# Performance work log

Hardware: AMD Instinct MI355X
Metric: run time of the kernel (lower is better)

Reference implementation:

```python
import jax, jax.numpy as jnp
import numpy as np

NEG_INF = -1e30  # safe stand-in for -inf so grads stay finite
LEAKY = 0.1      # leaky_hmm_coefficient passed to ChainFunction.apply

B, T, D = 32, 500, 2048   # batch, frames, num pdfs
S, E = 2048, 65536        # denominator graph: states, arcs


def setup_inputs() -> dict:
    key = jax.random.key(0)
    k1, k2, k3, k4, k5 = jax.random.split(key, 5)
    x = jax.random.normal(k1, (B, T, D), dtype=jnp.float32)  # nnet outputs (log-space)
    from_state = jax.random.randint(k2, (E,), 0, S)
    to_state = jax.random.randint(k3, (E,), 0, S)
    pdf_ids = jax.random.randint(k4, (E,), 0, D)
    # arc log-weights (negative, like normalized FST weights)
    log_weights = -2.0 * jax.random.uniform(k5, (E,), dtype=jnp.float32)
    log_init = jnp.full((S,), -np.log(float(S)), dtype=jnp.float32)   # uniform initial
    log_final = jnp.zeros((S,), dtype=jnp.float32)                    # all states final
    return {
        "x": x,
        "log_weights": log_weights,
        "log_init": log_init,
        "log_final": log_final,
        "from_state": from_state,
        "to_state": to_state,
        "pdf_ids": pdf_ids,
    }


def _segment_logsumexp(scores, seg_ids, num_segments):
    # scores: [E, B]; logsumexp per destination state -> [S, B]
    m = jax.ops.segment_max(scores, seg_ids, num_segments=num_segments)
    m = jnp.maximum(m, NEG_INF)  # empty segments -> finite sentinel
    sums = jax.ops.segment_sum(jnp.exp(scores - m[seg_ids]), seg_ids,
                               num_segments=num_segments)
    return m + jnp.log(jnp.maximum(sums, 1e-30))


def reference(x, log_weights, log_init, log_final, from_state, to_state, pdf_ids):
    # LF-MMI chain forward recursion (log domain) over the denominator graph,
    # with leaky-HMM transitions (prob. LEAKY of jumping to any state ~ init dist).
    Bv = x.shape[0]
    Sv = log_init.shape[0]
    log_leaky = jnp.log(jnp.float32(LEAKY))

    def step(alpha, xt):  # alpha: [S, B] log-probs, xt: [B, D]
        # leaky-HMM: alpha <- logaddexp(alpha, log_leaky + init * total_mass)
        tot = jax.scipy.special.logsumexp(alpha, axis=0)           # [B]
        alpha = jnp.logaddexp(alpha, log_leaky + log_init[:, None] + tot[None, :])
        # arc scores: alpha[src] + arc weight + frame pdf score
        scores = alpha[from_state] + log_weights[:, None] + xt[:, pdf_ids].T  # [E, B]
        new_alpha = _segment_logsumexp(scores, to_state, Sv)        # [S, B]
        return new_alpha, None

    alpha0 = jnp.broadcast_to(log_init[:, None], (Sv, Bv))
    alphaT, _ = jax.lax.scan(step, alpha0, jnp.swapaxes(x, 0, 1))  # scan over T
    objf = jax.scipy.special.logsumexp(alphaT + log_final[:, None], axis=0)  # [B]
    return -jnp.sum(objf)  # Energy returns -objf
```

## Files before the change

kernel.cpp:

```cpp
#include <hip/hip_runtime.h>
#include <cstdint>

#define NS 2048
#define NE 65536
#define ND 2048
#define NB 32
#define NT 500
#define NGROUPS 32
#define ELLCAP (2*NE)
#define LEAKYF 0.1f
#define NBG 16
#define NSP 16

#define WS_COUNTS 0
#define WS_CURSOR 8192
#define WS_WIDTHS 16384
#define WS_GBASE  16640
#define WS_ALBUF  20480
#define WS_ARC    544768

typedef float __attribute__((ext_vector_type(2))) f2v;

__device__ __forceinline__ void ld2_l3(const float2* p0, const float2* p1,
                                       float2& r0, float2& r1) {
    f2v a, b;
    asm volatile("global_load_dwordx2 %0, %2, off sc0 sc1\n\t"
                 "global_load_dwordx2 %1, %3, off sc0 sc1\n\t"
                 "s_waitcnt vmcnt(0)"
                 : "=&v"(a), "=&v"(b) : "v"(p0), "v"(p1) : "memory");
    r0 = make_float2(a.x, a.y); r1 = make_float2(b.x, b.y);
}
__device__ __forceinline__ void st2_l3(float2* p, float2 v) {
    f2v d; d.x = v.x; d.y = v.y;
    asm volatile("global_store_dwordx2 %0, %1, off sc0 sc1"
                 :: "v"(p), "v"(d) : "memory");
}

__global__ void k_init(const float* __restrict__ log_init, float* albuf, float* out,
                       uint32_t* counts, uint32_t* cursor, uint4* arcp) {
    int tid = blockIdx.x * blockDim.x + threadIdx.x;
    int n = blockDim.x * gridDim.x;
    for (int i = tid; i < NS; i += n) { counts[i] = 0u; cursor[i] = 0u; }
    for (int i = tid; i < ELLCAP; i += n) arcp[i] = make_uint4(0u, 0u, 0u, 0u);
    float2* ab = reinterpret_cast<float2*>(albuf);
    for (int i = tid; i < NBG * NS; i += n) {
        int s = i & (NS - 1);
        float a = __expf(log_init[s]);
        ab[i]            = make_float2(a, a);
        ab[NBG * NS + i] = make_float2(-1.f, -1.f);
    }
    if (tid == 0) out[0] = 0.0f;
}

__global__ void k_count(const int* __restrict__ to_state, uint32_t* counts) {
    int e = blockIdx.x * blockDim.x + threadIdx.x;
    if (e < NE) atomicAdd(&counts[to_state[e]], 1u);
}

__global__ void k_widths(const uint32_t* __restrict__ counts, uint32_t* widths, uint32_t* gbase) {
    int g = threadIdx.x;
    if (g < NGROUPS) {
        uint32_t w = 0u;
        for (int i = 0; i < 64; ++i) w = max(w, counts[g*64 + i]);
        widths[g] = w;
    }
    __syncthreads();
    if (threadIdx.x == 0) {
        uint32_t acc = 0u;
        for (int g2 = 0; g2 < NGROUPS; ++g2) { gbase[g2] = acc; acc += widths[g2] * 64u; }
        gbase[NGROUPS] = acc;
    }
}

__global__ void k_scatter(const int* __restrict__ from_state, const int* __restrict__ to_state,
                          const int* __restrict__ pdf_ids, const float* __restrict__ log_w,
                          const float* __restrict__ log_init,
                          const uint32_t* __restrict__ gbase, uint32_t* cursor, uint4* arcp) {
    int e = blockIdx.x * blockDim.x + threadIdx.x;
    if (e >= NE) return;
    int s = to_state[e];
    int g = s >> 6;
    uint32_t slot = atomicAdd(&cursor[s], 1u);
    uint32_t pos = gbase[g] + slot * 64u + (uint32_t)(s & 63);
    int fs = from_state[e];
    uint32_t meta = (uint32_t)fs | ((uint32_t)pdf_ids[e] << 16);
    float w  = __expf(log_w[e]);
    float w2 = LEAKYF * __expf(log_init[fs]) * w;
    arcp[pos] = make_uint4(meta, __float_as_uint(w), __float_as_uint(w2), 0u);
}

__global__ __launch_bounds__(1024, 1) void k_fwd(
    const float* __restrict__ x, const float* __restrict__ log_final,
    const uint4* __restrict__ arc, const uint32_t* __restrict__ widths,
    const uint32_t* __restrict__ gbase,
    float* albuf, float* out)
{
    __shared__ __align__(16) float2 e2[NS];
    __shared__ __align__(16) float2 Xs[2 * ND];
    __shared__ __align__(16) float2 pt[16 * 64];
    __shared__ __align__(16) float2 red[16];

    const int tid  = threadIdx.x;
    const int bg   = blockIdx.x & 15;
    const int sp   = blockIdx.x >> 4;
    const int lane = tid & 63;
    const int wid  = tid >> 6;
    const int gsel = wid >> 3;
    const int wsl  = wid & 7;
    const int g    = sp * 2 + gsel;

    const float* x0 = x + (size_t)(bg * 2)     * NT * ND;
    const float* x1 = x + (size_t)(bg * 2 + 1) * NT * ND;

    Xs[tid]        = make_float2(__expf(x0[tid]),        __expf(x1[tid]));
    Xs[tid + 1024] = make_float2(__expf(x0[tid + 1024]), __expf(x1[tid + 1024]));

    const int wd = (int)widths[g];
    const uint4* ap = arc + gbase[g] + lane;
    float2* albuf2 = reinterpret_cast<float2*>(albuf);

    float C0 = 0.f, C1 = 0.f;

    for (int t = 0; t < NT; ++t) {
        const int par = t & 1;
        const float2* cbuf = albuf2 + ((size_t)par * NBG + bg) * NS;
        float2*       nbuf = albuf2 + ((size_t)(par ^ 1) * NBG + bg) * NS;
        float2* Xcur = Xs + (size_t)par * ND;
        float2* Xnxt = Xs + (size_t)(par ^ 1) * ND;
        const uint32_t sexp = (uint32_t)((t >> 1) & 1);

        float2 A0, A1;
        for (;;) {
            ld2_l3(cbuf + tid, cbuf + tid + 1024, A0, A1);
            uint32_t m = ((__float_as_uint(A0.x) >> 31) ^ sexp)
                       | ((__float_as_uint(A0.y) >> 31) ^ sexp)
                       | ((__float_as_uint(A1.x) >> 31) ^ sexp)
                       | ((__float_as_uint(A1.y) >> 31) ^ sexp);
            if (m == 0u) break;
            __builtin_amdgcn_s_sleep(1);
        }
        A0.x = fabsf(A0.x); A0.y = fabsf(A0.y);
        A1.x = fabsf(A1.x); A1.y = fabsf(A1.y);

        float pa0, pa1, pb0, pb1;
        const bool pf = (t + 1 < NT);
        if (pf) {
            const size_t o = (size_t)(t + 1) * ND;
            pa0 = x0[o + tid];        pb0 = x1[o + tid];
            pa1 = x0[o + tid + 1024]; pb1 = x1[o + tid + 1024];
        }

        e2[tid]        = A0;
        e2[tid + 1024] = A1;
        float u0 = A0.x + A1.x, u1 = A0.y + A1.y;
        #pragma unroll
        for (int off = 32; off > 0; off >>= 1) {
            u0 += __shfl_down(u0, off, 64);
            u1 += __shfl_down(u1, off, 64);
        }
        if (lane == 0) red[wid] = make_float2(u0, u1);
        __syncthreads();

        float T0 = 0.f, T1 = 0.f;
        #pragma unroll
        for (int j = 0; j < 16; ++j) { float2 q = red[j]; T0 += q.x; T1 += q.y; }
        const float i0 = 1.0f / T0, i1 = 1.0f / T1;
        if (tid == 0) { C0 += __logf(T0); C1 += __logf(T1); }

        float2 acc = make_float2(0.f, 0.f);
        for (int i = wsl; i < wd; i += 8) {
            uint4 A = ap[(size_t)i * 64];
            const float w  = __uint_as_float(A.y);
            const float w2 = __uint_as_float(A.z);
            const int src = (int)(A.x & 0xFFFFu);
            const int pdf = (int)(A.x >> 16);
            float2 ev = e2[src];
            float2 xv = Xcur[pdf];
            acc.x = fmaf(xv.x, fmaf(ev.x * i0, w, w2), acc.x);
            acc.y = fmaf(xv.y, fmaf(ev.y * i1, w, w2), acc.y);
        }
        pt[wid * 64 + lane] = acc;
        if (pf) {
            Xnxt[tid]        = make_float2(__expf(pa0), __expf(pb0));
            Xnxt[tid + 1024] = make_float2(__expf(pa1), __expf(pb1));
        }
        __syncthreads();

        if (wsl == 0) {
            float2 r = pt[(gsel * 8) * 64 + lane];
            #pragma unroll
            for (int k = 1; k < 8; ++k) {
                float2 q = pt[(gsel * 8 + k) * 64 + lane];
                r.x += q.x; r.y += q.y;
            }
            const float sg = (((t + 1) >> 1) & 1) ? -1.f : 1.f;
            st2_l3(nbuf + sp * 128 + gsel * 64 + lane,
                   make_float2(r.x * sg, r.y * sg));
        }
    }

    if (sp == 0) {
        const float2* fbuf = albuf2 + (size_t)bg * NS;
        const uint32_t sexp = (uint32_t)((NT >> 1) & 1);
        float2 A0, A1;
        for (;;) {
            ld2_l3(fbuf + tid, fbuf + tid + 1024, A0, A1);
            uint32_t m = ((__float_as_uint(A0.x) >> 31) ^ sexp)
                       | ((__float_as_uint(A0.y) >> 31) ^ sexp)
                       | ((__float_as_uint(A1.x) >> 31) ^ sexp)
                       | ((__float_as_uint(A1.y) >> 31) ^ sexp);
            if (m == 0u) break;
            __builtin_amdgcn_s_sleep(1);
        }
        A0.x = fabsf(A0.x); A0.y = fabsf(A0.y);
        A1.x = fabsf(A1.x); A1.y = fabsf(A1.y);
        float f0 = __expf(log_final[tid]);
        float f1 = __expf(log_final[tid + 1024]);
        float u0 = A0.x * f0 + A1.x * f1;
        float u1 = A0.y * f0 + A1.y * f1;
        #pragma unroll
        for (int off = 32; off > 0; off >>= 1) {
            u0 += __shfl_down(u0, off, 64);
            u1 += __shfl_down(u1, off, 64);
        }
        if (lane == 0) red[wid] = make_float2(u0, u1);
        __syncthreads();
        if (tid == 0) {
            float t0 = 0.f, t1 = 0.f;
            #pragma unroll
            for (int j = 0; j < 16; ++j) { t0 += red[j].x; t1 += red[j].y; }
            atomicAdd(out, -(__logf(t0) + C0) - (__logf(t1) + C1));
        }
    }
}

extern "C" void kernel_launch(void* const* d_in, const int* in_sizes, int n_in,
                              void* d_out, int out_size, void* d_ws, size_t ws_size,
                              hipStream_t stream) {
    const float* x         = (const float*)d_in[0];
    const float* log_w     = (const float*)d_in[1];
    const float* log_init  = (const float*)d_in[2];
    const float* log_final = (const float*)d_in[3];
    const int*   from_st   = (const int*)d_in[4];
    const int*   to_st     = (const int*)d_in[5];
    const int*   pdf_ids   = (const int*)d_in[6];
    float* out = (float*)d_out;

    uint8_t* ws = (uint8_t*)d_ws;
    uint32_t* counts = (uint32_t*)(ws + WS_COUNTS);
    uint32_t* cursor = (uint32_t*)(ws + WS_CURSOR);
    uint32_t* widths = (uint32_t*)(ws + WS_WIDTHS);
    uint32_t* gbase  = (uint32_t*)(ws + WS_GBASE);
    float*    albuf  = (float*)(ws + WS_ALBUF);
    uint4*    arc    = (uint4*)(ws + WS_ARC);

    k_init   <<<512, 256, 0, stream>>>(log_init, albuf, out, counts, cursor, arc);
    k_count  <<<NE/256, 256, 0, stream>>>(to_st, counts);
    k_widths <<<1, 64, 0, stream>>>(counts, widths, gbase);
    k_scatter<<<NE/256, 256, 0, stream>>>(from_st, to_st, pdf_ids, log_w, log_init,
                                          gbase, cursor, arc);
    k_fwd    <<<NSP*NBG, 1024, 0, stream>>>(x, log_final, arc, widths, gbase,
                                            albuf, out);
}
```

Baseline: 2.010 ms.

## Interleave two independent batch chains per block to hide cross-block sync latency

Each persistent block now owns one 64-state group and handles two batch-pair chains in turn within every time step, instead of two state groups for one batch pair. While the block works on one chain, the other chain's alpha slice can be produced by the other blocks, so spin-wait time is meant to overlap with useful work. The grid stays at 256 blocks, now arranged as 32 state splits by 8 batch quads. This doubles the shared-memory X buffers and the number of block barriers per step, and each block writes 64 states per chain rather than 128.

```diff
diff --git a/kernel.cpp b/kernel.cpp
--- a/kernel.cpp
+++ b/kernel.cpp
@@ -9,8 +9,9 @@
 #define NGROUPS 32
 #define ELLCAP (2*NE)
 #define LEAKYF 0.1f
-#define NBG 16
-#define NSP 16
+#define NBQ 8
+#define NCH 2
+#define NSP 32
 
 #define WS_COUNTS 0
 #define WS_CURSOR 8192
@@ -35,6 +36,12 @@
     asm volatile("global_store_dwordx2 %0, %1, off sc0 sc1"
                  :: "v"(p), "v"(d) : "memory");
 }
+__device__ __forceinline__ uint32_t stale4(float2 A0, float2 A1, uint32_t sexp) {
+    return ((__float_as_uint(A0.x) >> 31) ^ sexp)
+         | ((__float_as_uint(A0.y) >> 31) ^ sexp)
+         | ((__float_as_uint(A1.x) >> 31) ^ sexp)
+         | ((__float_as_uint(A1.y) >> 31) ^ sexp);
+}
 
 __global__ void k_init(const float* __restrict__ log_init, float* albuf, float* out,
                        uint32_t* counts, uint32_t* cursor, uint4* arcp) {
@@ -43,11 +50,12 @@
     for (int i = tid; i < NS; i += n) { counts[i] = 0u; cursor[i] = 0u; }
     for (int i = tid; i < ELLCAP; i += n) arcp[i] = make_uint4(0u, 0u, 0u, 0u);
     float2* ab = reinterpret_cast<float2*>(albuf);
-    for (int i = tid; i < NBG * NS; i += n) {
+    const int PL = NBQ * NCH * NS;
+    for (int i = tid; i < PL; i += n) {
         int s = i & (NS - 1);
         float a = __expf(log_init[s]);
-        ab[i]            = make_float2(a, a);
-        ab[NBG * NS + i] = make_float2(-1.f, -1.f);
+        ab[i]      = make_float2(a, a);
+        ab[PL + i] = make_float2(-1.f, -1.f);
     }
     if (tid == 0) out[0] = 0.0f;
 }
@@ -96,141 +104,151 @@
     float* albuf, float* out)
 {
     __shared__ __align__(16) float2 e2[NS];
-    __shared__ __align__(16) float2 Xs[2 * ND];
+    __shared__ __align__(16) float2 Xs[NCH * 2 * ND];
     __shared__ __align__(16) float2 pt[16 * 64];
     __shared__ __align__(16) float2 red[16];
 
     const int tid  = threadIdx.x;
-    const int bg   = blockIdx.x & 15;
-    const int sp   = blockIdx.x >> 4;
+    const int bq   = blockIdx.x & 7;
+    const int sp   = blockIdx.x >> 3;
     const int lane = tid & 63;
     const int wid  = tid >> 6;
-    const int gsel = wid >> 3;
-    const int wsl  = wid & 7;
-    const int g    = sp * 2 + gsel;
-
-    const float* x0 = x + (size_t)(bg * 2)     * NT * ND;
-    const float* x1 = x + (size_t)(bg * 2 + 1) * NT * ND;
-
-    Xs[tid]        = make_float2(__expf(x0[tid]),        __expf(x1[tid]));
-    Xs[tid + 1024] = make_float2(__expf(x0[tid + 1024]), __expf(x1[tid + 1024]));
-
-    const int wd = (int)widths[g];
-    const uint4* ap = arc + gbase[g] + lane;
+
+    const float* xc0a = x + (size_t)(bq * 4 + 0) * NT * ND;
+    const float* xc0b = x + (size_t)(bq * 4 + 1) * NT * ND;
+    const float* xc1a = x + (size_t)(bq * 4 + 2) * NT * ND;
+    const float* xc1b = x + (size_t)(bq * 4 + 3) * NT * ND;
+
+    Xs[tid]              = make_float2(__expf(xc0a[tid]),        __expf(xc0b[tid]));
+    Xs[tid + 1024]       = make_float2(__expf(xc0a[tid + 1024]), __expf(xc0b[tid + 1024]));
+    Xs[2*ND + tid]        = make_float2(__expf(xc1a[tid]),        __expf(xc1b[tid]));
+    Xs[2*ND + tid + 1024] = make_float2(__expf(xc1a[tid + 1024]), __expf(xc1b[tid + 1024]));
+
+    const int wd = (int)widths[sp];
+    const uint4* ap = arc + gbase[sp] + lane;
     float2* albuf2 = reinterpret_cast<float2*>(albuf);
-
-    float C0 = 0.f, C1 = 0.f;
+    const int PL = NBQ * NCH * NS;
+
+    float Ca0 = 0.f, Ca1 = 0.f, Cb0 = 0.f, Cb1 = 0.f;
 
     for (int t = 0; t < NT; ++t) {
         const int par = t & 1;
-        const float2* cbuf = albuf2 + ((size_t)par * NBG + bg) * NS;
-        float2*       nbuf = albuf2 + ((size_t)(par ^ 1) * NBG + bg) * NS;
-        float2* Xcur = Xs + (size_t)par * ND;
-        float2* Xnxt = Xs + (size_t)(par ^ 1) * ND;
         const uint32_t sexp = (uint32_t)((t >> 1) & 1);
-
-        float2 A0, A1;
-        for (;;) {
-            ld2_l3(cbuf + tid, cbuf + tid + 1024, A0, A1);
-            uint32_t m = ((__float_as_uint(A0.x) >> 31) ^ sexp)
-                       | ((__float_as_uint(A0.y) >> 31) ^ sexp)
-                       | ((__float_as_uint(A1.x) >> 31) ^ sexp)
-                       | ((__float_as_uint(A1.y) >> 31) ^ sexp);
-            if (m == 0u) break;
-            __builtin_amdgcn_s_sleep(1);
+        const float sg = (((t + 1) >> 1) & 1) ? -1.f : 1.f;
+        const bool pf = (t + 1 < NT);
+
+        #pragma unroll
+        for (int ch = 0; ch < NCH; ++ch) {
+            const float2* cbuf = albuf2 + (size_t)par * PL + ((size_t)bq * NCH + ch) * NS;
+            float2*       nbuf = albuf2 + (size_t)(par ^ 1) * PL + ((size_t)bq * NCH + ch) * NS;
+            float2* Xcur = Xs + (size_t)(ch * 2 + par) * ND;
+            float2* Xnxt = Xs + (size_t)(ch * 2 + (par ^ 1)) * ND;
+            const float* xA = ch ? xc1a : xc0a;
+            const float* xB = ch ? xc1b : xc0b;
+
+            float2 A0, A1;
+            for (;;) {
+                ld2_l3(cbuf + tid, cbuf + tid + 1024, A0, A1);
+                if (stale4(A0, A1, sexp) == 0u) break;
+                __builtin_amdgcn_s_sleep(1);
+            }
+            A0.x = fabsf(A0.x); A0.y = fabsf(A0.y);
+            A1.x = fabsf(A1.x); A1.y = fabsf(A1.y);
+
+            float pa0, pa1, pb0, pb1;
+            if (pf) {
+                const size_t o = (size_t)(t + 1) * ND;
+                pa0 = xA[o + tid];        pb0 = xB[o + tid];
+                pa1 = xA[o + tid + 1024]; pb1 = xB[o + tid + 1024];
+            }
+
+            e2[tid]        = A0;
+            e2[tid + 1024] = A1;
+            float u0 = A0.x + A1.x, u1 = A0.y + A1.y;
+            #pragma unroll
+            for (int off = 32; off > 0; off >>= 1) {
+                u0 += __shfl_down(u0, off, 64);
+                u1 += __shfl_down(u1, off, 64);
+            }
+            if (lane == 0) red[wid] = make_float2(u0, u1);
+            __syncthreads();
+
+            float T0 = 0.f, T1 = 0.f;
+            #pragma unroll
+            for (int j = 0; j < 16; ++j) { float2 q = red[j]; T0 += q.x; T1 += q.y; }
+            const float i0 = 1.0f / T0, i1 = 1.0f / T1;
+            if (tid == 0) {
+                if (ch == 0) { Ca0 += __logf(T0); Ca1 += __logf(T1); }
+                else         { Cb0 += __logf(T0); Cb1 += __logf(T1); }
+            }
+
+            float2 acc = make_float2(0.f, 0.f);
+            for (int i = wid; i < wd; i += 16) {
+                uint4 A = ap[(size_t)i * 64];
+                const float w  = __uint_as_float(A.y);
+                const float w2 = __uint_as_float(A.z);
+                const int src = (int)(A.x & 0xFFFFu);
+                const int pdf = (int)(A.x >> 16);
+                float2 ev = e2[src];
+                float2 xv = Xcur[pdf];
+                acc.x = fmaf(xv.x, fmaf(ev.x * i0, w, w2), acc.x);
+                acc.y = fmaf(xv.y, fmaf(ev.y * i1, w, w2), acc.y);
+            }
+            pt[wid * 64 + lane] = acc;
+            if (pf) {
+                Xnxt[tid]        = make_float2(__expf(pa0), __expf(pb0));
+                Xnxt[tid + 1024] = make_float2(__expf(pa1), __expf(pb1));
+            }
+            __syncthreads();
+
+            if (wid == 0) {
+                float2 r = pt[lane];
+                #pragma unroll
+                for (int k = 1; k < 16; ++k) {
+                    float2 q = pt[k * 64 + lane];
+                    r.x += q.x; r.y += q.y;
+                }
+                st2_l3(nbuf + sp * 64 + lane, make_float2(r.x * sg, r.y * sg));
+            }
         }
-        A0.x = fabsf(A0.x); A0.y = fabsf(A0.y);
-        A1.x = fabsf(A1.x); A1.y = fabsf(A1.y);
-
-        float pa0, pa1, pb0, pb1;
-        const bool pf = (t + 1 < NT);
-        if (pf) {
-            const size_t o = (size_t)(t + 1) * ND;
-            pa0 = x0[o + tid];        pb0 = x1[o + tid];
-            pa1 = x0[o + tid + 1024]; pb1 = x1[o + tid + 1024];
+    }
+    __syncthreads();
+
+    if (sp == 0) {
+        const uint32_t sexp = (uint32_t)((NT >> 1) & 1);
+        float obj = 0.f;
+        #pragma unroll
+        for (int ch = 0; ch < NCH; ++ch) {
+            const float2* fbuf = albuf2 + ((size_t)bq * NCH + ch) * NS;
+            float2 A0, A1;
+            for (;;) {
+                ld2_l3(fbuf + tid, fbuf + tid + 1024, A0, A1);
+                if (stale4(A0, A1, sexp) == 0u) break;
+                __builtin_amdgcn_s_sleep(1);
+            }
+            A0.x = fabsf(A0.x); A0.y = fabsf(A0.y);
+            A1.x = fabsf(A1.x); A1.y = fabsf(A1.y);
+            float f0 = __expf(log_final[tid]);
+            float f1 = __expf(log_final[tid + 1024]);
+            float u0 = A0.x * f0 + A1.x * f1;
+            float u1 = A0.y * f0 + A1.y * f1;
+            #pragma unroll
+            for (int off = 32; off > 0; off >>= 1) {
+                u0 += __shfl_down(u0, off, 64);
+                u1 += __shfl_down(u1, off, 64);
+            }
+            if (lane == 0) red[wid] = make_float2(u0, u1);
+            __syncthreads();
+            if (tid == 0) {
+                float t0 = 0.f, t1 = 0.f;
+                #pragma unroll
+                for (int j = 0; j < 16; ++j) { t0 += red[j].x; t1 += red[j].y; }
+                if (ch == 0) obj += (__logf(t0) + Ca0) + (__logf(t1) + Ca1);
+                else         obj += (__logf(t0) + Cb0) + (__logf(t1) + Cb1);
+            }
+            __syncthreads();
         }
-
-        e2[tid]        = A0;
-        e2[tid + 1024] = A1;
-        float u0 = A0.x + A1.x, u1 = A0.y + A1.y;
-        #pragma unroll
-        for (int off = 32; off > 0; off >>= 1) {
-            u0 += __shfl_down(u0, off, 64);
-            u1 += __shfl_down(u1, off, 64);
-        }
-        if (lane == 0) red[wid] = make_float2(u0, u1);
-        __syncthreads();
-
-        float T0 = 0.f, T1 = 0.f;
-        #pragma unroll
-        for (int j = 0; j < 16; ++j) { float2 q = red[j]; T0 += q.x; T1 += q.y; }
-        const float i0 = 1.0f / T0, i1 = 1.0f / T1;
-        if (tid == 0) { C0 += __logf(T0); C1 += __logf(T1); }
-
-        float2 acc = make_float2(0.f, 0.f);
-        for (int i = wsl; i < wd; i += 8) {
-            uint4 A = ap[(size_t)i * 64];
-            const float w  = __uint_as_float(A.y);
-            const float w2 = __uint_as_float(A.z);
-            const int src = (int)(A.x & 0xFFFFu);
-            const int pdf = (int)(A.x >> 16);
-            float2 ev = e2[src];
-            float2 xv = Xcur[pdf];
-            acc.x = fmaf(xv.x, fmaf(ev.x * i0, w, w2), acc.x);
-            acc.y = fmaf(xv.y, fmaf(ev.y * i1, w, w2), acc.y);
-        }
-        pt[wid * 64 + lane] = acc;
-        if (pf) {
-            Xnxt[tid]        = make_float2(__expf(pa0), __expf(pb0));
-            Xnxt[tid + 1024] = make_float2(__expf(pa1), __expf(pb1));
-        }
-        __syncthreads();
-
-        if (wsl == 0) {
-            float2 r = pt[(gsel * 8) * 64 + lane];
-            #pragma unroll
-            for (int k = 1; k < 8; ++k) {
-                float2 q = pt[(gsel * 8 + k) * 64 + lane];
-                r.x += q.x; r.y += q.y;
-            }
-            const float sg = (((t + 1) >> 1) & 1) ? -1.f : 1.f;
-            st2_l3(nbuf + sp * 128 + gsel * 64 + lane,
-                   make_float2(r.x * sg, r.y * sg));
-        }
-    }
-
-    if (sp == 0) {
-        const float2* fbuf = albuf2 + (size_t)bg * NS;
-        const uint32_t sexp = (uint32_t)((NT >> 1) & 1);
-        float2 A0, A1;
-        for (;;) {
-            ld2_l3(fbuf + tid, fbuf + tid + 1024, A0, A1);
-            uint32_t m = ((__float_as_uint(A0.x) >> 31) ^ sexp)
-                       | ((__float_as_uint(A0.y) >> 31) ^ sexp)
-                       | ((__float_as_uint(A1.x) >> 31) ^ sexp)
-                       | ((__float_as_uint(A1.y) >> 31) ^ sexp);
-            if (m == 0u) break;
-            __builtin_amdgcn_s_sleep(1);
-        }
-        A0.x = fabsf(A0.x); A0.y = fabsf(A0.y);
-        A1.x = fabsf(A1.x); A1.y = fabsf(A1.y);
-        float f0 = __expf(log_final[tid]);
-        float f1 = __expf(log_final[tid + 1024]);
-        float u0 = A0.x * f0 + A1.x * f1;
-        float u1 = A0.y * f0 + A1.y * f1;
-        #pragma unroll
-        for (int off = 32; off > 0; off >>= 1) {
-            u0 += __shfl_down(u0, off, 64);
-            u1 += __shfl_down(u1, off, 64);
-        }
-        if (lane == 0) red[wid] = make_float2(u0, u1);
-        __syncthreads();
-        if (tid == 0) {
-            float t0 = 0.f, t1 = 0.f;
-            #pragma unroll
-            for (int j = 0; j < 16; ++j) { t0 += red[j].x; t1 += red[j].y; }
-            atomicAdd(out, -(__logf(t0) + C0) - (__logf(t1) + C1));
-        }
+        if (tid == 0) atomicAdd(out, -obj);
     }
 }
 
@@ -259,6 +277,6 @@
     k_widths <<<1, 64, 0, stream>>>(counts, widths, gbase);
     k_scatter<<<NE/256, 256, 0, stream>>>(from_st, to_st, pdf_ids, log_w, log_init,
                                           gbase, cursor, arc);
-    k_fwd    <<<NSP*NBG, 1024, 0, stream>>>(x, log_final, arc, widths, gbase,
+    k_fwd    <<<NSP*NBQ, 1024, 0, stream>>>(x, log_final, arc, widths, gbase,
                                             albuf, out);
 }
```

Result: slower. 2.199 ms (+9.4%).

## Split forward recursion across 512 smaller blocks, one state group each

Applied to the files above, without the earlier changes.

The persistent forward kernel moves from 256 blocks of 1024 threads, each handling two 64-state groups, to 512 blocks of 512 threads, each handling one group. The aim is to spread the per-step arc work over more CUs and shorten each block's critical path between the cross-block synchronisation points. Each block now polls and loads the full 2048-state alpha vector with four loads per thread. The cost is twice as much redundant alpha polling, exp of the x frame and shared-memory setup across blocks. It also needs all 512 blocks to be co-resident, or the spin-wait barrier can deadlock.

```diff
diff --git a/kernel.cpp b/kernel.cpp
--- a/kernel.cpp
+++ b/kernel.cpp
@@ -10,7 +10,7 @@
 #define ELLCAP (2*NE)
 #define LEAKYF 0.1f
 #define NBG 16
-#define NSP 16
+#define NSP 32
 
 #define WS_COUNTS 0
 #define WS_CURSOR 8192
@@ -21,19 +21,27 @@
 
 typedef float __attribute__((ext_vector_type(2))) f2v;
 
-__device__ __forceinline__ void ld2_l3(const float2* p0, const float2* p1,
-                                       float2& r0, float2& r1) {
-    f2v a, b;
-    asm volatile("global_load_dwordx2 %0, %2, off sc0 sc1\n\t"
-                 "global_load_dwordx2 %1, %3, off sc0 sc1\n\t"
+__device__ __forceinline__ void ld4_l3(const float2* p0, const float2* p1,
+                                       const float2* p2, const float2* p3,
+                                       float2& r0, float2& r1, float2& r2, float2& r3) {
+    f2v a, b, c, d;
+    asm volatile("global_load_dwordx2 %0, %4, off sc0 sc1\n\t"
+                 "global_load_dwordx2 %1, %5, off sc0 sc1\n\t"
+                 "global_load_dwordx2 %2, %6, off sc0 sc1\n\t"
+                 "global_load_dwordx2 %3, %7, off sc0 sc1\n\t"
                  "s_waitcnt vmcnt(0)"
-                 : "=&v"(a), "=&v"(b) : "v"(p0), "v"(p1) : "memory");
+                 : "=&v"(a), "=&v"(b), "=&v"(c), "=&v"(d)
+                 : "v"(p0), "v"(p1), "v"(p2), "v"(p3) : "memory");
     r0 = make_float2(a.x, a.y); r1 = make_float2(b.x, b.y);
+    r2 = make_float2(c.x, c.y); r3 = make_float2(d.x, d.y);
 }
 __device__ __forceinline__ void st2_l3(float2* p, float2 v) {
     f2v d; d.x = v.x; d.y = v.y;
     asm volatile("global_store_dwordx2 %0, %1, off sc0 sc1"
                  :: "v"(p), "v"(d) : "memory");
+}
+__device__ __forceinline__ uint32_t sgn(float v, uint32_t sexp) {
+    return (__float_as_uint(v) >> 31) ^ sexp;
 }
 
 __global__ void k_init(const float* __restrict__ log_init, float* albuf, float* out,
@@ -43,11 +51,12 @@
     for (int i = tid; i < NS; i += n) { counts[i] = 0u; cursor[i] = 0u; }
     for (int i = tid; i < ELLCAP; i += n) arcp[i] = make_uint4(0u, 0u, 0u, 0u);
     float2* ab = reinterpret_cast<float2*>(albuf);
-    for (int i = tid; i < NBG * NS; i += n) {
+    const int PL = NBG * NS;
+    for (int i = tid; i < PL; i += n) {
         int s = i & (NS - 1);
         float a = __expf(log_init[s]);
-        ab[i]            = make_float2(a, a);
-        ab[NBG * NS + i] = make_float2(-1.f, -1.f);
+        ab[i]      = make_float2(a, a);
+        ab[PL + i] = make_float2(-1.f, -1.f);
     }
     if (tid == 0) out[0] = 0.0f;
 }
@@ -89,7 +98,7 @@
     arcp[pos] = make_uint4(meta, __float_as_uint(w), __float_as_uint(w2), 0u);
 }
 
-__global__ __launch_bounds__(1024, 1) void k_fwd(
+__global__ __launch_bounds__(512, 4) void k_fwd(
     const float* __restrict__ x, const float* __restrict__ log_final,
     const uint4* __restrict__ arc, const uint32_t* __restrict__ widths,
     const uint32_t* __restrict__ gbase,
@@ -97,62 +106,72 @@
 {
     __shared__ __align__(16) float2 e2[NS];
     __shared__ __align__(16) float2 Xs[2 * ND];
-    __shared__ __align__(16) float2 pt[16 * 64];
-    __shared__ __align__(16) float2 red[16];
+    __shared__ __align__(16) float2 pt[8 * 64];
+    __shared__ __align__(16) float2 red[8];
 
     const int tid  = threadIdx.x;
     const int bg   = blockIdx.x & 15;
     const int sp   = blockIdx.x >> 4;
     const int lane = tid & 63;
     const int wid  = tid >> 6;
-    const int gsel = wid >> 3;
-    const int wsl  = wid & 7;
-    const int g    = sp * 2 + gsel;
 
     const float* x0 = x + (size_t)(bg * 2)     * NT * ND;
     const float* x1 = x + (size_t)(bg * 2 + 1) * NT * ND;
 
-    Xs[tid]        = make_float2(__expf(x0[tid]),        __expf(x1[tid]));
-    Xs[tid + 1024] = make_float2(__expf(x0[tid + 1024]), __expf(x1[tid + 1024]));
-
-    const int wd = (int)widths[g];
-    const uint4* ap = arc + gbase[g] + lane;
+    #pragma unroll
+    for (int k = 0; k < 4; ++k) {
+        int idx = tid + k * 512;
+        Xs[idx] = make_float2(__expf(x0[idx]), __expf(x1[idx]));
+    }
+
+    const int wd = (int)widths[sp];
+    const uint4* ap = arc + gbase[sp] + lane;
     float2* albuf2 = reinterpret_cast<float2*>(albuf);
+    const int PL = NBG * NS;
 
     float C0 = 0.f, C1 = 0.f;
 
     for (int t = 0; t < NT; ++t) {
         const int par = t & 1;
-        const float2* cbuf = albuf2 + ((size_t)par * NBG + bg) * NS;
-        float2*       nbuf = albuf2 + ((size_t)(par ^ 1) * NBG + bg) * NS;
+        const float2* cbuf = albuf2 + (size_t)par * PL + (size_t)bg * NS;
+        float2*       nbuf = albuf2 + (size_t)(par ^ 1) * PL + (size_t)bg * NS;
         float2* Xcur = Xs + (size_t)par * ND;
         float2* Xnxt = Xs + (size_t)(par ^ 1) * ND;
         const uint32_t sexp = (uint32_t)((t >> 1) & 1);
 
-        float2 A0, A1;
+        float2 A0, A1, A2, A3;
         for (;;) {
-            ld2_l3(cbuf + tid, cbuf + tid + 1024, A0, A1);
-            uint32_t m = ((__float_as_uint(A0.x) >> 31) ^ sexp)
-                       | ((__float_as_uint(A0.y) >> 31) ^ sexp)
-                       | ((__float_as_uint(A1.x) >> 31) ^ sexp)
-                       | ((__float_as_uint(A1.y) >> 31) ^ sexp);
+            ld4_l3(cbuf + tid, cbuf + tid + 512, cbuf + tid + 1024, cbuf + tid + 1536,
+                   A0, A1, A2, A3);
+            uint32_t m = sgn(A0.x, sexp) | sgn(A0.y, sexp)
+                       | sgn(A1.x, sexp) | sgn(A1.y, sexp)
+                       | sgn(A2.x, sexp) | sgn(A2.y, sexp)
+                       | sgn(A3.x, sexp) | sgn(A3.y, sexp);
             if (m == 0u) break;
             __builtin_amdgcn_s_sleep(1);
         }
         A0.x = fabsf(A0.x); A0.y = fabsf(A0.y);
         A1.x = fabsf(A1.x); A1.y = fabsf(A1.y);
-
-        float pa0, pa1, pb0, pb1;
+        A2.x = fabsf(A2.x); A2.y = fabsf(A2.y);
+        A3.x = fabsf(A3.x); A3.y = fabsf(A3.y);
+
+        float pa[4], pb[4];
         const bool pf = (t + 1 < NT);
         if (pf) {
             const size_t o = (size_t)(t + 1) * ND;
-            pa0 = x0[o + tid];        pb0 = x1[o + tid];
-            pa1 = x0[o + tid + 1024]; pb1 = x1[o + tid + 1024];
+            #pragma unroll
+            for (int k = 0; k < 4; ++k) {
+                pa[k] = x0[o + tid + k * 512];
+                pb[k] = x1[o + tid + k * 512];
+            }
         }
 
         e2[tid]        = A0;
-        e2[tid + 1024] = A1;
-        float u0 = A0.x + A1.x, u1 = A0.y + A1.y;
+        e2[tid + 512]  = A1;
+        e2[tid + 1024] = A2;
+        e2[tid + 1536] = A3;
+        float u0 = A0.x + A1.x + A2.x + A3.x;
+        float u1 = A0.y + A1.y + A2.y + A3.y;
         #pragma unroll
         for (int off = 32; off > 0; off >>= 1) {
             u0 += __shfl_down(u0, off, 64);
@@ -163,12 +182,12 @@
 
         float T0 = 0.f, T1 = 0.f;
         #pragma unroll
-        for (int j = 0; j < 16; ++j) { float2 q = red[j]; T0 += q.x; T1 += q.y; }
+        for (int j = 0; j < 8; ++j) { float2 q = red[j]; T0 += q.x; T1 += q.y; }
         const float i0 = 1.0f / T0, i1 = 1.0f / T1;
         if (tid == 0) { C0 += __logf(T0); C1 += __logf(T1); }
 
         float2 acc = make_float2(0.f, 0.f);
-        for (int i = wsl; i < wd; i += 8) {
+        for (int i = wid; i < wd; i += 8) {
             uint4 A = ap[(size_t)i * 64];
             const float w  = __uint_as_float(A.y);
             const float w2 = __uint_as_float(A.z);
@@ -181,43 +200,47 @@
         }
         pt[wid * 64 + lane] = acc;
         if (pf) {
-            Xnxt[tid]        = make_float2(__expf(pa0), __expf(pb0));
-            Xnxt[tid + 1024] = make_float2(__expf(pa1), __expf(pb1));
+            #pragma unroll
+            for (int k = 0; k < 4; ++k)
+                Xnxt[tid + k * 512] = make_float2(__expf(pa[k]), __expf(pb[k]));
         }
         __syncthreads();
 
-        if (wsl == 0) {
-            float2 r = pt[(gsel * 8) * 64 + lane];
+        if (wid == 0) {
+            float2 r = pt[lane];
             #pragma unroll
             for (int k = 1; k < 8; ++k) {
-                float2 q = pt[(gsel * 8 + k) * 64 + lane];
+                float2 q = pt[k * 64 + lane];
                 r.x += q.x; r.y += q.y;
             }
             const float sg = (((t + 1) >> 1) & 1) ? -1.f : 1.f;
-            st2_l3(nbuf + sp * 128 + gsel * 64 + lane,
-                   make_float2(r.x * sg, r.y * sg));
-        }
-    }
+            st2_l3(nbuf + sp * 64 + lane, make_float2(r.x * sg, r.y * sg));
+        }
+    }
+    __syncthreads();
 
     if (sp == 0) {
         const float2* fbuf = albuf2 + (size_t)bg * NS;
         const uint32_t sexp = (uint32_t)((NT >> 1) & 1);
-        float2 A0, A1;
+        float2 A0, A1, A2, A3;
         for (;;) {
-            ld2_l3(fbuf + tid, fbuf + tid + 1024, A0, A1);
-            uint32_t m = ((__float_as_uint(A0.x) >> 31) ^ sexp)
-                       | ((__float_as_uint(A0.y) >> 31) ^ sexp)
-                       | ((__float_as_uint(A1.x) >> 31) ^ sexp)
-                       | ((__float_as_uint(A1.y) >> 31) ^ sexp);
+            ld4_l3(fbuf + tid, fbuf + tid + 512, fbuf + tid + 1024, fbuf + tid + 1536,
+                   A0, A1, A2, A3);
+            uint32_t m = sgn(A0.x, sexp) | sgn(A0.y, sexp)
+                       | sgn(A1.x, sexp) | sgn(A1.y, sexp)
+                       | sgn(A2.x, sexp) | sgn(A2.y, sexp)
+                       | sgn(A3.x, sexp) | sgn(A3.y, sexp);
             if (m == 0u) break;
             __builtin_amdgcn_s_sleep(1);
         }
-        A0.x = fabsf(A0.x); A0.y = fabsf(A0.y);
-        A1.x = fabsf(A1.x); A1.y = fabsf(A1.y);
-        float f0 = __expf(log_final[tid]);
-        float f1 = __expf(log_final[tid + 1024]);
-        float u0 = A0.x * f0 + A1.x * f1;
-        float u1 = A0.y * f0 + A1.y * f1;
+        float u0 = 0.f, u1 = 0.f;
+        #pragma unroll
+        for (int k = 0; k < 4; ++k) {
+            float2 A = (k == 0) ? A0 : (k == 1) ? A1 : (k == 2) ? A2 : A3;
+            float f = __expf(log_final[tid + k * 512]);
+            u0 += fabsf(A.x) * f;
+            u1 += fabsf(A.y) * f;
+        }
         #pragma unroll
         for (int off = 32; off > 0; off >>= 1) {
             u0 += __shfl_down(u0, off, 64);
@@ -228,7 +251,7 @@
         if (tid == 0) {
             float t0 = 0.f, t1 = 0.f;
             #pragma unroll
-            for (int j = 0; j < 16; ++j) { t0 += red[j].x; t1 += red[j].y; }
+            for (int j = 0; j < 8; ++j) { t0 += red[j].x; t1 += red[j].y; }
             atomicAdd(out, -(__logf(t0) + C0) - (__logf(t1) + C1));
         }
     }
@@ -259,6 +282,6 @@
     k_widths <<<1, 64, 0, stream>>>(counts, widths, gbase);
     k_scatter<<<NE/256, 256, 0, stream>>>(from_st, to_st, pdf_ids, log_w, log_init,
                                           gbase, cursor, arc);
-    k_fwd    <<<NSP*NBG, 1024, 0, stream>>>(x, log_final, arc, widths, gbase,
-                                            albuf, out);
-}
+    k_fwd    <<<NSP*NBG, 512, 0, stream>>>(x, log_final, arc, widths, gbase,
+                                           albuf, out);
+}
```

Result: slower. 2.306 ms (+14.7%).
